# Kernel optimization log

Hardware: AMD Instinct MI355X
Metric: run time of the kernel (lower is better)

## Reference

```python
import math
import jax, jax.numpy as jnp
import numpy as np

B, T, J, EMBED, W = 16, 243, 17, 256, 3  # D = EMBED + 1 = 257, KW = 2*W+1 = 7


def log_map0_spatial(x):
    """Lorentz log map at origin (curvature 1), returning the spatial part.
    x: [..., d+1] points on the hyperboloid. Equals log_map0(x)[..., 1:]."""
    x_t = x[..., :1]
    x_s = x[..., 1:]
    xn = jnp.clip(jnp.linalg.norm(x_s, axis=-1, keepdims=True), 1e-7, None)
    return jnp.arccosh(jnp.maximum(x_t, 1.0 + 1e-7)) / xn * x_s


def exp_map0(v):
    """Lorentz exp map at origin. v: [..., d+1] tangent vector (time comp 0)."""
    v_s = v[..., 1:]
    n = jnp.clip(jnp.linalg.norm(v_s, axis=-1, keepdims=True), 1e-7, None)
    return jnp.concatenate([jnp.cosh(n), jnp.sinh(n) / n * v_s], axis=-1)


def setup_inputs() -> dict:
    key = jax.random.key(0)
    ks = jax.random.split(key, 8)
    # valid hyperboloid points: time = sqrt(1 + ||spatial||^2)
    s = jax.random.normal(ks[0], (B, T, J, EMBED), jnp.float32) * 0.5
    t = jnp.sqrt(1.0 + jnp.sum(s * s, axis=-1, keepdims=True))
    x_seq = jnp.concatenate([t, s], axis=-1)  # [B,T,J,D]
    vel_seq = jax.random.normal(ks[1], (B, T, J, EMBED + 1), jnp.float32) * 0.1
    sc = 1.0 / math.sqrt(EMBED)
    Wq = jax.random.normal(ks[2], (EMBED, EMBED), jnp.float32) * sc
    Wk = jax.random.normal(ks[3], (EMBED, EMBED), jnp.float32) * sc
    Wv = jax.random.normal(ks[4], (EMBED, EMBED), jnp.float32) * sc
    bq = jax.random.normal(ks[5], (EMBED,), jnp.float32) * sc
    bk = jax.random.normal(ks[6], (EMBED,), jnp.float32) * sc
    bv = jax.random.normal(ks[7], (EMBED,), jnp.float32) * sc
    tau = jnp.ones((1,), jnp.float32)
    return {"x_seq": x_seq, "vel_seq": vel_seq, "tau": tau,
            "Wq": Wq, "bq": bq, "Wk": Wk, "bk": bk, "Wv": Wv, "bv": bv}


def reference(x_seq, vel_seq, tau, Wq, bq, Wk, bk, Wv, bv):
    Bb, Tt, Jj, D = x_seq.shape
    d = D - 1
    KW = 2 * W + 1
    # [B,T,J,D] -> [B*J, T, D]
    x_flat = jnp.transpose(x_seq, (0, 2, 1, 3)).reshape(Bb * Jj, Tt, D)
    spatial = log_map0_spatial(x_flat)  # [BJ, T, d]
    q = spatial @ Wq.T + bq
    k = spatial @ Wk.T + bk
    v = spatial @ Wv.T + bv
    # replicate-pad along time, build +/-W windows (fixed small loop over KW=7)
    k_pad = jnp.pad(k, ((0, 0), (W, W), (0, 0)), mode='edge')
    v_pad = jnp.pad(v, ((0, 0), (W, W), (0, 0)), mode='edge')
    k_win = jnp.stack([k_pad[:, i:i + Tt] for i in range(KW)], axis=2)  # [BJ,T,KW,d]
    v_win = jnp.stack([v_pad[:, i:i + Tt] for i in range(KW)], axis=2)
    tau_c = jnp.maximum(tau, 0.001)  # shape [1], broadcasts
    logits = jnp.einsum('btd,btwd->btw', q, k_win) / (math.sqrt(d) * tau_c)
    # mask out-of-range frames at the temporal boundaries
    frame_idx = jnp.arange(Tt)[:, None] + (jnp.arange(KW) - W)[None, :]
    boundary = (frame_idx < 0) | (frame_idx >= Tt)  # [T,KW]
    logits = jnp.where(boundary[None], -jnp.inf, logits)
    attn = jax.nn.softmax(logits, axis=-1)  # [BJ,T,KW]
    agg = jnp.einsum('btw,btwd->btd', attn, v_win)  # [BJ,T,d]
    agg_full = jnp.pad(agg, ((0, 0), (0, 0), (1, 0)))  # prepend zero time comp
    z = exp_map0(agg_full)  # [BJ,T,D]
    return jnp.transpose(z.reshape(Bb, Jj, Tt, D), (0, 2, 1, 3))
```

## Files before the change

kernel.cpp:

```cpp
#include <hip/hip_runtime.h>
#include <hip/hip_bf16.h>

#define B_   16
#define T_   243
#define J_   17
#define E_   256
#define D_   257
#define BJ_  (B_ * J_)
#define M_   (BJ_ * T_)

typedef __bf16 bf16x8 __attribute__((ext_vector_type(8)));
typedef float  f32x4  __attribute__((ext_vector_type(4)));

static __device__ __forceinline__ float bf2f(unsigned short u) {
  unsigned int v = ((unsigned int)u) << 16;
  return __builtin_bit_cast(float, v);
}
static __device__ __forceinline__ unsigned short f2bf(float f) {
  __hip_bfloat16 h = __float2bfloat16(f);
  return __builtin_bit_cast(unsigned short, h);
}
static __device__ __forceinline__ float wave_sum(float v) {
  v += __shfl_xor(v, 1);
  v += __shfl_xor(v, 2);
  v += __shfl_xor(v, 4);
  v += __shfl_xor(v, 8);
  v += __shfl_xor(v, 16);
  v += __shfl_xor(v, 32);
  return v;
}
static __device__ __forceinline__ void gload_lds16(const void* g, void* l) {
  __builtin_amdgcn_global_load_lds(
      (const __attribute__((address_space(1))) void*)g,
      (__attribute__((address_space(3))) void*)l, 16, 0, 0);
}

__global__ void fuse_w_kernel(const float* __restrict__ Wq,
                              const float* __restrict__ Wk,
                              const float* __restrict__ Wv,
                              __hip_bfloat16* __restrict__ wf) {
  int idx = blockIdx.x * 256 + threadIdx.x;
  float v = (idx < 65536) ? Wq[idx]
          : (idx < 131072) ? Wk[idx - 65536]
                           : Wv[idx - 131072];
  ((unsigned short*)wf)[idx] = f2bf(v);
}

__global__ __launch_bounds__(256) void qkv_gemm_kernel(
    const float* __restrict__ x, const unsigned short* __restrict__ Wf,
    const float* __restrict__ bq, const float* __restrict__ bk,
    const float* __restrict__ bv, unsigned short* __restrict__ C) {
  __shared__ __align__(16) unsigned short lA[64 * 256];
  __shared__ __align__(16) unsigned short lW[2][128 * 64];

  int tid  = threadIdx.x;
  int w    = tid >> 6;
  int lane = tid & 63;
  int wr   = w >> 1;
  int wcn  = w & 1;
  int m0   = blockIdx.x * 64;

  {
    char* bA = (char*)lA;
    for (int rr = 0; rr < 16; ++rr) {
      int lr = w * 16 + rr;
      int m  = m0 + lr; if (m > M_ - 1) m = M_ - 1;
      int bj = m / T_;  int t = m - bj * T_;
      int b  = bj / J_; int j = bj - b * J_;
      const float* row = x + (size_t)((b * T_ + t) * J_ + j) * D_;
      float xs[4], ss = 0.f;
#pragma unroll
      for (int i = 0; i < 4; ++i) {
        xs[i] = row[1 + lane * 4 + i];
        ss += xs[i] * xs[i];
      }
      ss = wave_sum(ss);
      float xn = fmaxf(sqrtf(ss), 1e-7f);
      float alpha = acoshf(fmaxf(row[0], 1.f + 1e-7f)) / xn;
      ushort4 o;
      o.x = f2bf(xs[0] * alpha); o.y = f2bf(xs[1] * alpha);
      o.z = f2bf(xs[2] * alpha); o.w = f2bf(xs[3] * alpha);
      int byte = lr * 512 + ((lane * 8) ^ ((lr & 7) << 4));
      *(ushort4*)(bA + byte) = o;
    }
  }
  __syncthreads();

  int rowInWave = lane >> 3;
  int srcSlot   = (lane & 7) ^ rowInWave;

  const char* bA = (const char*)lA;

  for (int nt = 0; nt < 6; ++nt) {
    int n0 = nt * 128;

    float bias[4];
#pragma unroll
    for (int ni = 0; ni < 4; ++ni) {
      int colg = n0 + wcn * 64 + ni * 16 + (lane & 15);
      bias[ni] = (colg < 256) ? bq[colg]
               : (colg < 512) ? bk[colg - 256] : bv[colg - 512];
    }

    f32x4 acc[2][4] = {};

#pragma unroll
    for (int i = 0; i < 4; ++i) {
      int rbase = (w * 4 + i) * 8;
      gload_lds16(Wf + (size_t)(n0 + rbase + rowInWave) * 256 + srcSlot * 8,
                  lW[0] + rbase * 64);
    }
    __syncthreads();

    for (int kk = 0; kk < 4; ++kk) {
      if (kk < 3) {
#pragma unroll
        for (int i = 0; i < 4; ++i) {
          int rbase = (w * 4 + i) * 8;
          gload_lds16(Wf + (size_t)(n0 + rbase + rowInWave) * 256 +
                          (kk + 1) * 64 + srcSlot * 8,
                      lW[(kk + 1) & 1] + rbase * 64);
        }
      }
      const char* bW = (const char*)lW[kk & 1];
#pragma unroll
      for (int ki = 0; ki < 2; ++ki) {
        bf16x8 a[2], bfr[4];
        int cbA = kk * 128 + ki * 64 + (lane >> 4) * 16;
#pragma unroll
        for (int mi = 0; mi < 2; ++mi) {
          int r = wr * 32 + mi * 16 + (lane & 15);
          a[mi] = *(const bf16x8*)(bA + r * 512 + (cbA ^ ((r & 7) << 4)));
        }
        int cbB = ki * 64 + (lane >> 4) * 16;
#pragma unroll
        for (int ni = 0; ni < 4; ++ni) {
          int r = wcn * 64 + ni * 16 + (lane & 15);
          bfr[ni] = *(const bf16x8*)(bW + r * 128 + (cbB ^ ((r & 7) << 4)));
        }
#pragma unroll
        for (int mi = 0; mi < 2; ++mi)
#pragma unroll
          for (int ni = 0; ni < 4; ++ni)
            acc[mi][ni] = __builtin_amdgcn_mfma_f32_16x16x32_bf16(
                a[mi], bfr[ni], acc[mi][ni], 0, 0, 0);
      }
      __syncthreads();
    }

    char* bC = (char*)lW[0];
#pragma unroll
    for (int mi = 0; mi < 2; ++mi)
#pragma unroll
      for (int ni = 0; ni < 4; ++ni) {
        int col = wcn * 64 + ni * 16 + (lane & 15);
#pragma unroll
        for (int r = 0; r < 4; ++r) {
          int row  = wr * 32 + mi * 16 + (lane >> 4) * 4 + r;
          int byte = row * 256 + ((col * 2) ^ ((row & 7) << 4));
          *(unsigned short*)(bC + byte) = f2bf(acc[mi][ni][r] + bias[ni]);
        }
      }
    __syncthreads();
#pragma unroll
    for (int p = 0; p < 4; ++p) {
      int row  = p * 16 + (tid >> 4);
      int seg  = tid & 15;
      int byte = row * 256 + ((seg * 16) ^ ((row & 7) << 4));
      uint4 val = *(const uint4*)(bC + byte);
      int gm = m0 + row;
      if (gm < M_)
        *(uint4*)(C + (size_t)gm * 768 + n0 + seg * 8) = val;
    }
    __syncthreads();
  }
}

__global__ __launch_bounds__(256) void attn_kernel(
    const unsigned short* __restrict__ qkv, const float* __restrict__ tau,
    float* __restrict__ out) {
  int wid  = threadIdx.x >> 6;
  int lane = threadIdx.x & 63;
  int c  = blockIdx.x * 4 + wid;
  int t0 = c * 16;
  int t1 = min(T_, t0 + 16);
  int bj = blockIdx.y;
  int b = bj / J_, j = bj % J_;
  const unsigned short* base = qkv + (size_t)bj * T_ * 768;

  float tauc = fmaxf(tau[0], 1e-3f);
  float sc = 1.f / (16.f * tauc);

  for (int t = t0; t < t1; ++t) {
    ushort4 qa = *(const ushort4*)(base + (size_t)t * 768 + lane * 4);
    ushort4 ka[7], va[7];
#pragma unroll
    for (int ww = 0; ww < 7; ++ww) {
      int t2 = t + ww - 3;
      int tc = min(max(t2, 0), T_ - 1);
      const unsigned short* rowp = base + (size_t)tc * 768;
      ka[ww] = *(const ushort4*)(rowp + 256 + lane * 4);
      va[ww] = *(const ushort4*)(rowp + 512 + lane * 4);
    }
    float q0 = bf2f(qa.x), q1 = bf2f(qa.y), q2 = bf2f(qa.z), q3 = bf2f(qa.w);

    float logit[7];
#pragma unroll
    for (int ww = 0; ww < 7; ++ww) {
      float p = q0 * bf2f(ka[ww].x) + q1 * bf2f(ka[ww].y) +
                q2 * bf2f(ka[ww].z) + q3 * bf2f(ka[ww].w);
      p = wave_sum(p) * sc;
      int t2 = t + ww - 3;
      logit[ww] = (t2 < 0 || t2 >= T_) ? -INFINITY : p;
    }

    float mx = logit[0];
#pragma unroll
    for (int ww = 1; ww < 7; ++ww) mx = fmaxf(mx, logit[ww]);
    float e[7], s = 0.f;
#pragma unroll
    for (int ww = 0; ww < 7; ++ww) {
      e[ww] = expf(logit[ww] - mx);
      s += e[ww];
    }
    float inv = 1.f / s;

    float ag0 = 0.f, ag1 = 0.f, ag2 = 0.f, ag3 = 0.f;
#pragma unroll
    for (int ww = 0; ww < 7; ++ww) {
      ag0 += e[ww] * bf2f(va[ww].x);
      ag1 += e[ww] * bf2f(va[ww].y);
      ag2 += e[ww] * bf2f(va[ww].z);
      ag3 += e[ww] * bf2f(va[ww].w);
    }
    ag0 *= inv; ag1 *= inv; ag2 *= inv; ag3 *= inv;

    float nn = wave_sum(ag0*ag0 + ag1*ag1 + ag2*ag2 + ag3*ag3);
    float n = fmaxf(sqrtf(nn), 1e-7f);
    float scale = sinhf(n) / n;

    float* orow = out + ((size_t)(b * T_ + t) * J_ + j) * D_;
    if (lane == 0) orow[0] = coshf(n);
    float4 o; o.x = ag0 * scale; o.y = ag1 * scale;
    o.z = ag2 * scale; o.w = ag3 * scale;
    *(float4*)(orow + 1 + lane * 4) = o;
  }
}

extern "C" void kernel_launch(void* const* d_in, const int* in_sizes, int n_in,
                              void* d_out, int out_size, void* d_ws, size_t ws_size,
                              hipStream_t stream) {
  const float* x   = (const float*)d_in[0];
  const float* tau = (const float*)d_in[2];
  const float* Wq  = (const float*)d_in[3];
  const float* bq  = (const float*)d_in[4];
  const float* Wk  = (const float*)d_in[5];
  const float* bk  = (const float*)d_in[6];
  const float* Wv  = (const float*)d_in[7];
  const float* bv  = (const float*)d_in[8];
  float* out = (float*)d_out;

  char* ws = (char*)d_ws;
  __hip_bfloat16* wf  = (__hip_bfloat16*)(ws);
  unsigned short* qkv = (unsigned short*)(ws + 393216);

  fuse_w_kernel<<<dim3(768), dim3(256), 0, stream>>>(Wq, Wk, Wv, wf);
  qkv_gemm_kernel<<<dim3(1034), dim3(256), 0, stream>>>(
      x, (const unsigned short*)wf, bq, bk, bv, qkv);
  attn_kernel<<<dim3(4, BJ_), dim3(256), 0, stream>>>(qkv, tau, out);
}
```

Before: 321.6 us.

## Fold Wq·Wk into Gram matrix and fuse projections with windowed attention

Precomputes G = Wq^T Wk and bias-correction vectors, so logits become s_t^T G s_t' plus rank-one bias terms. This removes the separate Q and K projections and fuses the log-map, V projection, logits and softmax aggregation into one kernel per time chunk, with a 3-frame halo kept in LDS. The goal is to cut the GEMM FLOPs and avoid the round trip of the bf16 QKV buffer through global memory. In exchange, halo rows are recomputed per chunk, weights are read straight from global without LDS staging, and rounding G to bf16 adds some precision loss.

New measurement: 349.2 us. 8.6% more time.

```diff
diff --git a/kernel.cpp b/kernel.cpp
--- a/kernel.cpp
+++ b/kernel.cpp
@@ -4,10 +4,10 @@
 #define B_   16
 #define T_   243
 #define J_   17
-#define E_   256
-#define D_   257
 #define BJ_  (B_ * J_)
-#define M_   (BJ_ * T_)
+#define NCH  8
+#define TC   32
+#define KVR  48
 
 typedef __bf16 bf16x8 __attribute__((ext_vector_type(8)));
 typedef float  f32x4  __attribute__((ext_vector_type(4)));
@@ -21,229 +21,244 @@
   return __builtin_bit_cast(unsigned short, h);
 }
 static __device__ __forceinline__ float wave_sum(float v) {
-  v += __shfl_xor(v, 1);
-  v += __shfl_xor(v, 2);
-  v += __shfl_xor(v, 4);
-  v += __shfl_xor(v, 8);
-  v += __shfl_xor(v, 16);
-  v += __shfl_xor(v, 32);
+  v += __shfl_xor(v, 1);  v += __shfl_xor(v, 2);  v += __shfl_xor(v, 4);
+  v += __shfl_xor(v, 8);  v += __shfl_xor(v, 16); v += __shfl_xor(v, 32);
   return v;
 }
-static __device__ __forceinline__ void gload_lds16(const void* g, void* l) {
-  __builtin_amdgcn_global_load_lds(
-      (const __attribute__((address_space(1))) void*)g,
-      (__attribute__((address_space(3))) void*)l, 16, 0, 0);
-}
-
-__global__ void fuse_w_kernel(const float* __restrict__ Wq,
-                              const float* __restrict__ Wk,
-                              const float* __restrict__ Wv,
-                              __hip_bfloat16* __restrict__ wf) {
+
+__global__ void wv_kernel(const float* __restrict__ Wv,
+                          unsigned short* __restrict__ wv) {
   int idx = blockIdx.x * 256 + threadIdx.x;
-  float v = (idx < 65536) ? Wq[idx]
-          : (idx < 131072) ? Wk[idx - 65536]
-                           : Wv[idx - 131072];
-  ((unsigned short*)wf)[idx] = f2bf(v);
-}
-
-__global__ __launch_bounds__(256) void qkv_gemm_kernel(
-    const float* __restrict__ x, const unsigned short* __restrict__ Wf,
+  wv[idx] = f2bf(Wv[idx]);
+}
+
+__global__ __launch_bounds__(256) void gram_kernel(
+    const float* __restrict__ Wq, const float* __restrict__ Wk,
+    unsigned short* __restrict__ gt) {
+  int d = blockIdx.x, c = threadIdx.x;
+  float acc = 0.f;
+#pragma unroll 8
+  for (int i = 0; i < 256; ++i)
+    acc += Wq[i * 256 + c] * Wk[i * 256 + d];
+  gt[d * 256 + c] = f2bf(acc);
+}
+
+__global__ __launch_bounds__(256) void wvec_kernel(
+    const float* __restrict__ Wq, const float* __restrict__ Wk,
     const float* __restrict__ bq, const float* __restrict__ bk,
-    const float* __restrict__ bv, unsigned short* __restrict__ C) {
-  __shared__ __align__(16) unsigned short lA[64 * 256];
-  __shared__ __align__(16) unsigned short lW[2][128 * 64];
-
-  int tid  = threadIdx.x;
-  int w    = tid >> 6;
-  int lane = tid & 63;
-  int wr   = w >> 1;
-  int wcn  = w & 1;
-  int m0   = blockIdx.x * 64;
+    float* __restrict__ w1v, float* __restrict__ w2v,
+    float* __restrict__ bqkp) {
+  __shared__ float red[4];
+  int c = threadIdx.x;
+  float a1 = 0.f, a2 = 0.f;
+#pragma unroll 8
+  for (int i = 0; i < 256; ++i) {
+    a1 += Wk[i * 256 + c] * bq[i];
+    a2 += Wq[i * 256 + c] * bk[i];
+  }
+  w1v[c] = a1;
+  w2v[c] = a2;
+  float p = wave_sum(bq[c] * bk[c]);
+  if ((c & 63) == 0) red[c >> 6] = p;
+  __syncthreads();
+  if (c == 0) bqkp[0] = red[0] + red[1] + red[2] + red[3];
+}
+
+__global__ __launch_bounds__(256) void fused_kernel(
+    const float* __restrict__ x, const unsigned short* __restrict__ wv,
+    const unsigned short* __restrict__ gt, const float* __restrict__ w1v,
+    const float* __restrict__ w2v, const float* __restrict__ bqkp,
+    const float* __restrict__ bv, const float* __restrict__ tau,
+    float* __restrict__ out) {
+  __shared__ __align__(16) unsigned short sS[KVR * 256];
+  __shared__ __align__(16) unsigned short vL[KVR * 264];
+  __shared__ __align__(16) unsigned short sG[TC * 256];
+  __shared__ __align__(16) float Sb[TC * 52];
+  __shared__ float beta1[KVR], beta2[KVR];
+
+  int tid = threadIdx.x, w = tid >> 6, lane = tid & 63;
+  int ch = blockIdx.x, bj = blockIdx.y;
+  int b = bj / J_, j = bj % J_;
+  int t0 = ch * TC;
+
+  float isc = 1.f / (16.f * fmaxf(tau[0], 1e-3f));
+  float bqk = bqkp[0];
+  float4 w1r = *(const float4*)(w1v + lane * 4);
+  float4 w2r = *(const float4*)(w2v + lane * 4);
+
+  char* sB = (char*)sS;
+  char* gB = (char*)sG;
+
+  for (int rr = 0; rr < 12; ++rr) {
+    int r = w * 12 + rr;
+    int ts = t0 - 3 + r;
+    ts = min(max(ts, 0), T_ - 1);
+    const float* xr = x + ((size_t)((b * T_ + ts) * J_ + j)) * 257;
+    float xs0 = xr[1 + lane * 4], xs1 = xr[2 + lane * 4];
+    float xs2 = xr[3 + lane * 4], xs3 = xr[4 + lane * 4];
+    float ss = xs0 * xs0 + xs1 * xs1 + xs2 * xs2 + xs3 * xs3;
+    float s1 = w1r.x * xs0 + w1r.y * xs1 + w1r.z * xs2 + w1r.w * xs3;
+    float s2 = w2r.x * xs0 + w2r.y * xs1 + w2r.z * xs2 + w2r.w * xs3;
+#pragma unroll
+    for (int sh = 1; sh < 64; sh <<= 1) {
+      ss += __shfl_xor(ss, sh);
+      s1 += __shfl_xor(s1, sh);
+      s2 += __shfl_xor(s2, sh);
+    }
+    float xn = fmaxf(sqrtf(ss), 1e-7f);
+    float alpha = acoshf(fmaxf(xr[0], 1.f + 1e-7f)) / xn;
+    ushort4 o;
+    o.x = f2bf(xs0 * alpha); o.y = f2bf(xs1 * alpha);
+    o.z = f2bf(xs2 * alpha); o.w = f2bf(xs3 * alpha);
+    *(ushort4*)(sB + r * 512 + ((lane * 8) ^ ((r & 7) << 4))) = o;
+    if (lane == 0) { beta1[r] = alpha * s1; beta2[r] = alpha * s2; }
+  }
+  __syncthreads();
+
+  int fr = lane & 15, fq = lane >> 4;
+  int nb = w * 64;
 
   {
-    char* bA = (char*)lA;
-    for (int rr = 0; rr < 16; ++rr) {
-      int lr = w * 16 + rr;
-      int m  = m0 + lr; if (m > M_ - 1) m = M_ - 1;
-      int bj = m / T_;  int t = m - bj * T_;
-      int b  = bj / J_; int j = bj - b * J_;
-      const float* row = x + (size_t)((b * T_ + t) * J_ + j) * D_;
-      float xs[4], ss = 0.f;
-#pragma unroll
-      for (int i = 0; i < 4; ++i) {
-        xs[i] = row[1 + lane * 4 + i];
-        ss += xs[i] * xs[i];
+    f32x4 av[3][4] = {};
+#pragma unroll
+    for (int kk = 0; kk < 8; ++kk) {
+      bf16x8 bfr[4];
+#pragma unroll
+      for (int ni = 0; ni < 4; ++ni)
+        bfr[ni] = *(const bf16x8*)(wv + (size_t)(nb + ni * 16 + fr) * 256 +
+                                   kk * 32 + fq * 8);
+      bf16x8 a[3];
+#pragma unroll
+      for (int mi = 0; mi < 3; ++mi) {
+        int r = mi * 16 + fr;
+        a[mi] = *(const bf16x8*)(sB + r * 512 +
+                                 ((kk * 64 + fq * 16) ^ ((r & 7) << 4)));
       }
-      ss = wave_sum(ss);
-      float xn = fmaxf(sqrtf(ss), 1e-7f);
-      float alpha = acoshf(fmaxf(row[0], 1.f + 1e-7f)) / xn;
-      ushort4 o;
-      o.x = f2bf(xs[0] * alpha); o.y = f2bf(xs[1] * alpha);
-      o.z = f2bf(xs[2] * alpha); o.w = f2bf(xs[3] * alpha);
-      int byte = lr * 512 + ((lane * 8) ^ ((lr & 7) << 4));
-      *(ushort4*)(bA + byte) = o;
-    }
-  }
-  __syncthreads();
-
-  int rowInWave = lane >> 3;
-  int srcSlot   = (lane & 7) ^ rowInWave;
-
-  const char* bA = (const char*)lA;
-
-  for (int nt = 0; nt < 6; ++nt) {
-    int n0 = nt * 128;
-
-    float bias[4];
+#pragma unroll
+      for (int mi = 0; mi < 3; ++mi)
+#pragma unroll
+        for (int ni = 0; ni < 4; ++ni)
+          av[mi][ni] = __builtin_amdgcn_mfma_f32_16x16x32_bf16(
+              a[mi], bfr[ni], av[mi][ni], 0, 0, 0);
+    }
 #pragma unroll
     for (int ni = 0; ni < 4; ++ni) {
-      int colg = n0 + wcn * 64 + ni * 16 + (lane & 15);
-      bias[ni] = (colg < 256) ? bq[colg]
-               : (colg < 512) ? bk[colg - 256] : bv[colg - 512];
-    }
-
-    f32x4 acc[2][4] = {};
-
-#pragma unroll
-    for (int i = 0; i < 4; ++i) {
-      int rbase = (w * 4 + i) * 8;
-      gload_lds16(Wf + (size_t)(n0 + rbase + rowInWave) * 256 + srcSlot * 8,
-                  lW[0] + rbase * 64);
-    }
-    __syncthreads();
-
-    for (int kk = 0; kk < 4; ++kk) {
-      if (kk < 3) {
-#pragma unroll
-        for (int i = 0; i < 4; ++i) {
-          int rbase = (w * 4 + i) * 8;
-          gload_lds16(Wf + (size_t)(n0 + rbase + rowInWave) * 256 +
-                          (kk + 1) * 64 + srcSlot * 8,
-                      lW[(kk + 1) & 1] + rbase * 64);
+      int col = nb + ni * 16 + fr;
+      float bb = bv[col];
+#pragma unroll
+      for (int mi = 0; mi < 3; ++mi)
+#pragma unroll
+        for (int r2 = 0; r2 < 4; ++r2) {
+          int tr = mi * 16 + fq * 4 + r2;
+          vL[tr * 264 + col] = f2bf(av[mi][ni][r2] + bb);
         }
+    }
+  }
+
+  {
+    f32x4 ag[2][4] = {};
+#pragma unroll
+    for (int kk = 0; kk < 8; ++kk) {
+      bf16x8 bfr[4];
+#pragma unroll
+      for (int ni = 0; ni < 4; ++ni)
+        bfr[ni] = *(const bf16x8*)(gt + (size_t)(nb + ni * 16 + fr) * 256 +
+                                   kk * 32 + fq * 8);
+      bf16x8 a[2];
+#pragma unroll
+      for (int mi = 0; mi < 2; ++mi) {
+        int r = 3 + mi * 16 + fr;
+        a[mi] = *(const bf16x8*)(sB + r * 512 +
+                                 ((kk * 64 + fq * 16) ^ ((r & 7) << 4)));
       }
-      const char* bW = (const char*)lW[kk & 1];
-#pragma unroll
-      for (int ki = 0; ki < 2; ++ki) {
-        bf16x8 a[2], bfr[4];
-        int cbA = kk * 128 + ki * 64 + (lane >> 4) * 16;
-#pragma unroll
-        for (int mi = 0; mi < 2; ++mi) {
-          int r = wr * 32 + mi * 16 + (lane & 15);
-          a[mi] = *(const bf16x8*)(bA + r * 512 + (cbA ^ ((r & 7) << 4)));
+#pragma unroll
+      for (int mi = 0; mi < 2; ++mi)
+#pragma unroll
+        for (int ni = 0; ni < 4; ++ni)
+          ag[mi][ni] = __builtin_amdgcn_mfma_f32_16x16x32_bf16(
+              a[mi], bfr[ni], ag[mi][ni], 0, 0, 0);
+    }
+#pragma unroll
+    for (int ni = 0; ni < 4; ++ni) {
+      int d = nb + ni * 16 + fr;
+#pragma unroll
+      for (int mi = 0; mi < 2; ++mi)
+#pragma unroll
+        for (int r2 = 0; r2 < 4; ++r2) {
+          int qr = mi * 16 + fq * 4 + r2;
+          *(unsigned short*)(gB + qr * 512 + ((d * 2) ^ ((qr & 7) << 4))) =
+              f2bf(ag[mi][ni][r2]);
         }
-        int cbB = ki * 64 + (lane >> 4) * 16;
-#pragma unroll
-        for (int ni = 0; ni < 4; ++ni) {
-          int r = wcn * 64 + ni * 16 + (lane & 15);
-          bfr[ni] = *(const bf16x8*)(bW + r * 128 + (cbB ^ ((r & 7) << 4)));
-        }
-#pragma unroll
-        for (int mi = 0; mi < 2; ++mi)
-#pragma unroll
-          for (int ni = 0; ni < 4; ++ni)
-            acc[mi][ni] = __builtin_amdgcn_mfma_f32_16x16x32_bf16(
-                a[mi], bfr[ni], acc[mi][ni], 0, 0, 0);
-      }
-      __syncthreads();
-    }
-
-    char* bC = (char*)lW[0];
-#pragma unroll
-    for (int mi = 0; mi < 2; ++mi)
-#pragma unroll
-      for (int ni = 0; ni < 4; ++ni) {
-        int col = wcn * 64 + ni * 16 + (lane & 15);
-#pragma unroll
-        for (int r = 0; r < 4; ++r) {
-          int row  = wr * 32 + mi * 16 + (lane >> 4) * 4 + r;
-          int byte = row * 256 + ((col * 2) ^ ((row & 7) << 4));
-          *(unsigned short*)(bC + byte) = f2bf(acc[mi][ni][r] + bias[ni]);
-        }
-      }
-    __syncthreads();
-#pragma unroll
-    for (int p = 0; p < 4; ++p) {
-      int row  = p * 16 + (tid >> 4);
-      int seg  = tid & 15;
-      int byte = row * 256 + ((seg * 16) ^ ((row & 7) << 4));
-      uint4 val = *(const uint4*)(bC + byte);
-      int gm = m0 + row;
-      if (gm < M_)
-        *(uint4*)(C + (size_t)gm * 768 + n0 + seg * 8) = val;
-    }
-    __syncthreads();
-  }
-}
-
-__global__ __launch_bounds__(256) void attn_kernel(
-    const unsigned short* __restrict__ qkv, const float* __restrict__ tau,
-    float* __restrict__ out) {
-  int wid  = threadIdx.x >> 6;
-  int lane = threadIdx.x & 63;
-  int c  = blockIdx.x * 4 + wid;
-  int t0 = c * 16;
-  int t1 = min(T_, t0 + 16);
-  int bj = blockIdx.y;
-  int b = bj / J_, j = bj % J_;
-  const unsigned short* base = qkv + (size_t)bj * T_ * 768;
-
-  float tauc = fmaxf(tau[0], 1e-3f);
-  float sc = 1.f / (16.f * tauc);
-
-  for (int t = t0; t < t1; ++t) {
-    ushort4 qa = *(const ushort4*)(base + (size_t)t * 768 + lane * 4);
-    ushort4 ka[7], va[7];
-#pragma unroll
-    for (int ww = 0; ww < 7; ++ww) {
-      int t2 = t + ww - 3;
-      int tc = min(max(t2, 0), T_ - 1);
-      const unsigned short* rowp = base + (size_t)tc * 768;
-      ka[ww] = *(const ushort4*)(rowp + 256 + lane * 4);
-      va[ww] = *(const ushort4*)(rowp + 512 + lane * 4);
-    }
-    float q0 = bf2f(qa.x), q1 = bf2f(qa.y), q2 = bf2f(qa.z), q3 = bf2f(qa.w);
-
-    float logit[7];
-#pragma unroll
-    for (int ww = 0; ww < 7; ++ww) {
-      float p = q0 * bf2f(ka[ww].x) + q1 * bf2f(ka[ww].y) +
-                q2 * bf2f(ka[ww].z) + q3 * bf2f(ka[ww].w);
-      p = wave_sum(p) * sc;
-      int t2 = t + ww - 3;
-      logit[ww] = (t2 < 0 || t2 >= T_) ? -INFINITY : p;
-    }
-
-    float mx = logit[0];
-#pragma unroll
-    for (int ww = 1; ww < 7; ++ww) mx = fmaxf(mx, logit[ww]);
-    float e[7], s = 0.f;
-#pragma unroll
-    for (int ww = 0; ww < 7; ++ww) {
-      e[ww] = expf(logit[ww] - mx);
-      s += e[ww];
-    }
-    float inv = 1.f / s;
-
-    float ag0 = 0.f, ag1 = 0.f, ag2 = 0.f, ag3 = 0.f;
-#pragma unroll
-    for (int ww = 0; ww < 7; ++ww) {
-      ag0 += e[ww] * bf2f(va[ww].x);
-      ag1 += e[ww] * bf2f(va[ww].y);
-      ag2 += e[ww] * bf2f(va[ww].z);
-      ag3 += e[ww] * bf2f(va[ww].w);
-    }
-    ag0 *= inv; ag1 *= inv; ag2 *= inv; ag3 *= inv;
-
-    float nn = wave_sum(ag0*ag0 + ag1*ag1 + ag2*ag2 + ag3*ag3);
-    float n = fmaxf(sqrtf(nn), 1e-7f);
-    float scale = sinhf(n) / n;
-
-    float* orow = out + ((size_t)(b * T_ + t) * J_ + j) * D_;
-    if (lane == 0) orow[0] = coshf(n);
-    float4 o; o.x = ag0 * scale; o.y = ag1 * scale;
-    o.z = ag2 * scale; o.w = ag3 * scale;
-    *(float4*)(orow + 1 + lane * 4) = o;
+    }
+  }
+  __syncthreads();
+
+  for (int idx = w; idx < 6; idx += 4) {
+    int mi = idx / 3, nj = idx % 3;
+    f32x4 acc = {};
+#pragma unroll
+    for (int kk = 0; kk < 8; ++kk) {
+      int ra = mi * 16 + fr;
+      bf16x8 a = *(const bf16x8*)(gB + ra * 512 +
+                                  ((kk * 64 + fq * 16) ^ ((ra & 7) << 4)));
+      int rb = nj * 16 + fr;
+      bf16x8 bb = *(const bf16x8*)(sB + rb * 512 +
+                                   ((kk * 64 + fq * 16) ^ ((rb & 7) << 4)));
+      acc = __builtin_amdgcn_mfma_f32_16x16x32_bf16(a, bb, acc, 0, 0, 0);
+    }
+#pragma unroll
+    for (int r2 = 0; r2 < 4; ++r2) {
+      int qr = mi * 16 + fq * 4 + r2;
+      int tp = nj * 16 + fr;
+      Sb[qr * 52 + tp] = (acc[r2] + beta1[tp] + beta2[3 + qr] + bqk) * isc;
+    }
+  }
+  __syncthreads();
+
+  for (int rr = 0; rr < 8; ++rr) {
+    int qt = w * 8 + rr;
+    int t = t0 + qt;
+    if (t >= T_) break;
+
+    float pw[7];
+    float mx = -1e30f;
+#pragma unroll
+    for (int k7 = 0; k7 < 7; ++k7) {
+      int frame = t + k7 - 3;
+      float lg = (frame >= 0 && frame < T_) ? Sb[qt * 52 + qt + k7] : -1e30f;
+      pw[k7] = lg;
+      mx = fmaxf(mx, lg);
+    }
+    float sum = 0.f;
+#pragma unroll
+    for (int k7 = 0; k7 < 7; ++k7) {
+      float e = expf(pw[k7] - mx);
+      pw[k7] = e;
+      sum += e;
+    }
+    float inv = 1.f / sum;
+
+    float a0 = 0.f, a1 = 0.f, a2 = 0.f, a3 = 0.f;
+#pragma unroll
+    for (int k7 = 0; k7 < 7; ++k7) {
+      ushort4 vv = *(const ushort4*)(vL + (qt + k7) * 264 + lane * 4);
+      a0 += pw[k7] * bf2f(vv.x);
+      a1 += pw[k7] * bf2f(vv.y);
+      a2 += pw[k7] * bf2f(vv.z);
+      a3 += pw[k7] * bf2f(vv.w);
+    }
+    a0 *= inv; a1 *= inv; a2 *= inv; a3 *= inv;
+
+    float nn = wave_sum(a0 * a0 + a1 * a1 + a2 * a2 + a3 * a3);
+    float norm = fmaxf(sqrtf(nn), 1e-7f);
+    float sc2 = sinhf(norm) / norm;
+
+    float* orow = out + ((size_t)((b * T_ + t) * J_ + j)) * 257;
+    orow[1 + lane * 4] = a0 * sc2;
+    orow[2 + lane * 4] = a1 * sc2;
+    orow[3 + lane * 4] = a2 * sc2;
+    orow[4 + lane * 4] = a3 * sc2;
+    if (lane == 0) orow[0] = coshf(norm);
   }
 }
 
@@ -261,11 +276,15 @@
   float* out = (float*)d_out;
 
   char* ws = (char*)d_ws;
-  __hip_bfloat16* wf  = (__hip_bfloat16*)(ws);
-  unsigned short* qkv = (unsigned short*)(ws + 393216);
-
-  fuse_w_kernel<<<dim3(768), dim3(256), 0, stream>>>(Wq, Wk, Wv, wf);
-  qkv_gemm_kernel<<<dim3(1034), dim3(256), 0, stream>>>(
-      x, (const unsigned short*)wf, bq, bk, bv, qkv);
-  attn_kernel<<<dim3(4, BJ_), dim3(256), 0, stream>>>(qkv, tau, out);
-}
+  unsigned short* wv  = (unsigned short*)(ws);
+  unsigned short* gtb = (unsigned short*)(ws + 131072);
+  float* w1v  = (float*)(ws + 262144);
+  float* w2v  = (float*)(ws + 263168);
+  float* bqkp = (float*)(ws + 264192);
+
+  wv_kernel<<<dim3(256), dim3(256), 0, stream>>>(Wv, wv);
+  gram_kernel<<<dim3(256), dim3(256), 0, stream>>>(Wq, Wk, gtb);
+  wvec_kernel<<<dim3(1), dim3(256), 0, stream>>>(Wq, Wk, bq, bk, w1v, w2v, bqkp);
+  fused_kernel<<<dim3(NCH, BJ_), dim3(256), 0, stream>>>(
+      x, wv, gtb, w1v, w2v, bqkp, bv, tau, out);
+}
```
